# Performance work log

Measured on AMD Instinct MI355X. Metric: run time of the kernel, lower is better.

Reference implementation:

```python
import jax, jax.numpy as jnp
import numpy as np


def _conv1x1(W, b, x):
    # 1x1 conv == per-pixel matmul over channels: (O,C) x (B,C,H,W) -> (B,O,H,W)
    return jnp.einsum('oc,bchw->bohw', W, x) + b[None, :, None, None]


def setup_inputs() -> dict:
    key = jax.random.key(0)
    ks = jax.random.split(key, 7)
    B, C, H, W = 4, 256, 64, 64
    Cq = C // 8  # 32
    scale_qk = 1.0 / np.sqrt(C)
    x = jax.random.normal(ks[0], (B, C, H, W), dtype=jnp.float32)
    Wq = jax.random.normal(ks[1], (Cq, C), dtype=jnp.float32) * scale_qk
    bq = jnp.zeros((Cq,), dtype=jnp.float32)
    Wk = jax.random.normal(ks[2], (Cq, C), dtype=jnp.float32) * scale_qk
    bk = jnp.zeros((Cq,), dtype=jnp.float32)
    Wv = jax.random.normal(ks[3], (C, C), dtype=jnp.float32) * scale_qk
    bv = jnp.zeros((C,), dtype=jnp.float32)
    gamma = jnp.ones((1,), dtype=jnp.float32)  # torch init is 0; use 1 so attn branch is exercised
    return {'x': x, 'Wq': Wq, 'bq': bq, 'Wk': Wk, 'bk': bk, 'Wv': Wv, 'bv': bv, 'gamma': gamma}


def reference(x, Wq, bq, Wk, bk, Wv, bv, gamma):
    B, C, H, W = x.shape
    N = H * W
    # query/key projections + activation (relu), flattened over spatial dims
    q = jax.nn.relu(_conv1x1(Wq, bq, x)).reshape(B, -1, N)  # (B, C/8, N)
    k = jax.nn.relu(_conv1x1(Wk, bk, x)).reshape(B, -1, N)  # (B, C/8, N)
    # energy[b,n,m] = sum_c q[b,c,n] * k[b,c,m]  (= proj_query^T @ proj_key)
    energy = jnp.einsum('bcn,bcm->bnm', q, k)               # (B, N, N)
    attention = jax.nn.softmax(energy, axis=-1)
    v = jax.nn.relu(_conv1x1(Wv, bv, x)).reshape(B, C, N)   # (B, C, N)
    # out = v @ attention^T : out[b,c,n] = sum_m v[b,c,m] * attention[b,n,m]
    out = jnp.einsum('bcm,bnm->bcn', v, attention).reshape(B, C, H, W)
    out = gamma[0] * out + x
    return (out, attention)
```

## Files before the change

kernel.cpp:

```cpp
#include <hip/hip_runtime.h>
#include <hip/hip_bf16.h>

#define NB 4
#define NC 256
#define NQ 32
#define NN 4096
#define LOG2E 1.4426950408889634f

typedef __attribute__((ext_vector_type(4))) float f32x4;
typedef __attribute__((ext_vector_type(8))) short s16x8;

#define MFMA16(a, b, c) __builtin_amdgcn_mfma_f32_16x16x32_bf16((a), (b), (c), 0, 0, 0)

__device__ __forceinline__ float fexp2(float x) {
    float r;
    asm("v_exp_f32 %0, %1" : "=v"(r) : "v"(x));
    return r;
}

__device__ __forceinline__ void block_sync_lds() {
    asm volatile("s_waitcnt lgkmcnt(0)" ::: "memory");
    __builtin_amdgcn_s_barrier();
}

__device__ __forceinline__ int pswz(int row, int col) {
    return row * 64 + (col ^ ((row & 7) << 3));
}

__global__ __launch_bounds__(512, 2) void k_proj(
    const float* __restrict__ x,
    const float* __restrict__ Wq, const float* __restrict__ bq,
    const float* __restrict__ Wk, const float* __restrict__ bk,
    const float* __restrict__ Wv, const float* __restrict__ bv,
    __hip_bfloat16* __restrict__ qh, __hip_bfloat16* __restrict__ ql,
    __hip_bfloat16* __restrict__ kh, __hip_bfloat16* __restrict__ kl,
    __hip_bfloat16* __restrict__ vo)
{
    __shared__ __align__(16) float xs[NC * 64];
    const int b  = blockIdx.y;
    const int n0 = blockIdx.x * 64;
    const int t  = threadIdx.x;

    {
        const float* xb = x + (size_t)b * NC * NN + n0;
        #pragma unroll
        for (int it = 0; it < 8; ++it) {
            int i4 = t + it * 512;
            int c  = i4 >> 4;
            int nq = (i4 & 15) << 2;
            float4 v4 = *(const float4*)(xb + (size_t)c * NN + nq);
            *(float4*)&xs[c * 64 + nq] = v4;
        }
    }
    __syncthreads();

    const int g  = t >> 4;
    const int n4 = (t & 15) << 2;

    const float* Wr[10];
    float a[10][4];
    #pragma unroll
    for (int j = 0; j < 10; ++j) {
        int o = g + 32 * j;
        const float* Wrow; float bias;
        if (o < 32)      { Wrow = Wq + o * NC;        bias = bq[o]; }
        else if (o < 64) { Wrow = Wk + (o - 32) * NC; bias = bk[o - 32]; }
        else             { Wrow = Wv + (o - 64) * NC; bias = bv[o - 64]; }
        Wr[j] = Wrow;
        a[j][0] = a[j][1] = a[j][2] = a[j][3] = bias;
    }

    #pragma unroll 2
    for (int c0 = 0; c0 < NC; c0 += 4) {
        float4 xv[4];
        #pragma unroll
        for (int i = 0; i < 4; ++i) xv[i] = *(const float4*)&xs[(c0 + i) * 64 + n4];
        #pragma unroll
        for (int j = 0; j < 10; ++j) {
            float4 w = *(const float4*)(Wr[j] + c0);
            a[j][0] += w.x * xv[0].x + w.y * xv[1].x + w.z * xv[2].x + w.w * xv[3].x;
            a[j][1] += w.x * xv[0].y + w.y * xv[1].y + w.z * xv[2].y + w.w * xv[3].y;
            a[j][2] += w.x * xv[0].z + w.y * xv[1].z + w.z * xv[2].z + w.w * xv[3].z;
            a[j][3] += w.x * xv[0].w + w.y * xv[1].w + w.z * xv[2].w + w.w * xv[3].w;
        }
    }

    #pragma unroll
    for (int j = 0; j < 10; ++j) {
        int o = g + 32 * j;
        float a0 = fmaxf(a[j][0], 0.f), a1 = fmaxf(a[j][1], 0.f);
        float a2 = fmaxf(a[j][2], 0.f), a3 = fmaxf(a[j][3], 0.f);
        int nn = n0 + n4;
        if (o < 64) {
            __hip_bfloat16 *dh, *dl; int c; float sc;
            if (o < 32) { dh = qh; dl = ql; c = o;      sc = LOG2E; }
            else        { dh = kh; dl = kl; c = o - 32; sc = 1.0f;  }
            float vals[4] = {a0 * sc, a1 * sc, a2 * sc, a3 * sc};
            #pragma unroll
            for (int i = 0; i < 4; ++i) {
                float vv = vals[i];
                __hip_bfloat16 h = __float2bfloat16(vv);
                float lo = vv - __bfloat162float(h);
                size_t base = ((size_t)b * NN + nn + i) * NQ + c;
                dh[base] = h;
                dl[base] = __float2bfloat16(lo);
            }
        } else {
            union { __hip_bfloat16 h[4]; unsigned long long u; } pk;
            pk.h[0] = __float2bfloat16(a0); pk.h[1] = __float2bfloat16(a1);
            pk.h[2] = __float2bfloat16(a2); pk.h[3] = __float2bfloat16(a3);
            *(unsigned long long*)(vo + ((size_t)b * NC + (o - 64)) * NN + nn) = pk.u;
        }
    }
}

__global__ __launch_bounds__(1024, 4) void k_fused(
    const __hip_bfloat16* __restrict__ qh, const __hip_bfloat16* __restrict__ ql,
    const __hip_bfloat16* __restrict__ kh, const __hip_bfloat16* __restrict__ kl,
    const __hip_bfloat16* __restrict__ v,
    const float* __restrict__ x, const float* __restrict__ gamma,
    float* __restrict__ out, float* __restrict__ att)
{
    __shared__ __align__(16) __hip_bfloat16 ps[2][64 * 64];
    __shared__ float redM[16][16], redS[16][16];
    __shared__ float finM[64], finI[64];

    const int bid  = blockIdx.x;
    const int flat = (bid & 7) * 32 + (bid >> 3);
    const int b    = flat >> 6;
    const int n0   = (flat & 63) * 64;

    const int t = threadIdx.x, wv = t >> 6, lane = t & 63;
    const int r = lane & 15, hi = lane >> 4, kc = hi * 8;

    const __hip_bfloat16* khb = kh + (size_t)b * NN * NQ;
    const __hip_bfloat16* klb = kl + (size_t)b * NN * NQ;
    const __hip_bfloat16* vb  = v  + (size_t)b * NC * NN;

    {
        const int nt1 = wv >> 2, mq = wv & 3;
        const int nw = n0 + nt1 * 16;
        const s16x8 aqh = *(const s16x8*)(qh + ((size_t)b * NN + nw + r) * NQ + kc);
        const s16x8 aql = *(const s16x8*)(ql + ((size_t)b * NN + nw + r) * NQ + kc);
        const int mb = mq * 1024;
        float M = -3.0e38f, S = 0.f;
        s16x8 c0h = *(const s16x8*)(khb + (size_t)(mb + r) * NQ + kc);
        s16x8 c0l = *(const s16x8*)(klb + (size_t)(mb + r) * NQ + kc);
        s16x8 c1h = *(const s16x8*)(khb + (size_t)(mb + 16 + r) * NQ + kc);
        s16x8 c1l = *(const s16x8*)(klb + (size_t)(mb + 16 + r) * NQ + kc);
        #pragma unroll 1
        for (int it = 0; it < 32; ++it) {
            s16x8 u0h = c0h, u0l = c0l, u1h = c1h, u1l = c1l;
            if (it < 31) {
                int m = mb + (it + 1) * 32;
                c0h = *(const s16x8*)(khb + (size_t)(m + r) * NQ + kc);
                c0l = *(const s16x8*)(klb + (size_t)(m + r) * NQ + kc);
                c1h = *(const s16x8*)(khb + (size_t)(m + 16 + r) * NQ + kc);
                c1l = *(const s16x8*)(klb + (size_t)(m + 16 + r) * NQ + kc);
            }
            f32x4 e0 = {0.f, 0.f, 0.f, 0.f}, e1 = {0.f, 0.f, 0.f, 0.f};
            e0 = MFMA16(u0h, aqh, e0); e0 = MFMA16(u0l, aqh, e0); e0 = MFMA16(u0h, aql, e0);
            e1 = MFMA16(u1h, aqh, e1); e1 = MFMA16(u1l, aqh, e1); e1 = MFMA16(u1h, aql, e1);
            float mx = fmaxf(fmaxf(fmaxf(e0[0], e0[1]), fmaxf(e0[2], e0[3])),
                             fmaxf(fmaxf(e1[0], e1[1]), fmaxf(e1[2], e1[3])));
            float nm = fmaxf(M, mx);
            float s8 = fexp2(e0[0] - nm) + fexp2(e0[1] - nm) +
                       fexp2(e0[2] - nm) + fexp2(e0[3] - nm) +
                       fexp2(e1[0] - nm) + fexp2(e1[1] - nm) +
                       fexp2(e1[2] - nm) + fexp2(e1[3] - nm);
            S = S * fexp2(M - nm) + s8;
            M = nm;
        }
        #pragma unroll
        for (int off = 16; off <= 32; off <<= 1) {
            float M2 = __shfl_xor(M, off), S2 = __shfl_xor(S, off);
            float nm = fmaxf(M, M2);
            S = S * fexp2(M - nm) + S2 * fexp2(M2 - nm);
            M = nm;
        }
        if (lane < 16) { redM[wv][r] = M; redS[wv][r] = S; }
    }
    __syncthreads();
    if (t < 64) {
        const int w0 = (t >> 4) * 4, tl = t & 15;
        float M = redM[w0][tl], S = redS[w0][tl];
        #pragma unroll
        for (int i = 1; i < 4; ++i) {
            float M2 = redM[w0 + i][tl], S2 = redS[w0 + i][tl];
            float nm = fmaxf(M, M2);
            S = S * fexp2(M - nm) + S2 * fexp2(M2 - nm);
            M = nm;
        }
        finM[t] = M; finI[t] = 1.0f / S;
    }
    __syncthreads();

    if (wv < 8) {
        const int nt = wv >> 1, mh = wv & 1;
        const int nw = n0 + nt * 16;
        const s16x8 aqh = *(const s16x8*)(qh + ((size_t)b * NN + nw + r) * NQ + kc);
        const s16x8 aql = *(const s16x8*)(ql + ((size_t)b * NN + nw + r) * NQ + kc);
        const float fM = finM[nt * 16 + r], fI = finI[nt * 16 + r];
        float* arow = att + ((size_t)b * NN + nw + r) * NN;
        const int prow = nt * 16 + r;
        const int pc0  = mh * 32 + hi * 4;

        int mt = mh * 32;
        s16x8 c0h = *(const s16x8*)(khb + (size_t)(mt + r) * NQ + kc);
        s16x8 c0l = *(const s16x8*)(klb + (size_t)(mt + r) * NQ + kc);
        s16x8 c1h = *(const s16x8*)(khb + (size_t)(mt + 16 + r) * NQ + kc);
        s16x8 c1l = *(const s16x8*)(klb + (size_t)(mt + 16 + r) * NQ + kc);

        #pragma unroll 1
        for (int st = 0; st < 64; ++st) {
            const int buf = st & 1;
            s16x8 u0h = c0h, u0l = c0l, u1h = c1h, u1l = c1l;
            if (st < 63) {
                int mn = mt + 64;
                c0h = *(const s16x8*)(khb + (size_t)(mn + r) * NQ + kc);
                c0l = *(const s16x8*)(klb + (size_t)(mn + r) * NQ + kc);
                c1h = *(const s16x8*)(khb + (size_t)(mn + 16 + r) * NQ + kc);
                c1l = *(const s16x8*)(klb + (size_t)(mn + 16 + r) * NQ + kc);
            }
            f32x4 e0 = {0.f, 0.f, 0.f, 0.f}, e1 = {0.f, 0.f, 0.f, 0.f};
            e0 = MFMA16(u0h, aqh, e0); e0 = MFMA16(u0l, aqh, e0); e0 = MFMA16(u0h, aql, e0);
            e1 = MFMA16(u1h, aqh, e1); e1 = MFMA16(u1l, aqh, e1); e1 = MFMA16(u1h, aql, e1);

            f32x4 w0, w1;
            #pragma unroll
            for (int j = 0; j < 4; ++j) {
                w0[j] = fexp2(e0[j] - fM) * fI;
                w1[j] = fexp2(e1[j] - fM) * fI;
            }
            __builtin_nontemporal_store(w0, (f32x4*)(arow + mt + hi * 4));
            __builtin_nontemporal_store(w1, (f32x4*)(arow + mt + 16 + hi * 4));
            union { __hip_bfloat16 h[4]; unsigned long long u; } pk0, pk1;
            #pragma unroll
            for (int j = 0; j < 4; ++j) {
                pk0.h[j] = __float2bfloat16(w0[j]);
                pk1.h[j] = __float2bfloat16(w1[j]);
            }
            *(unsigned long long*)&ps[buf][pswz(prow, pc0)]      = pk0.u;
            *(unsigned long long*)&ps[buf][pswz(prow, pc0 + 16)] = pk1.u;

            block_sync_lds();
            mt += 64;
        }
    } else {
        const int cw = (wv - 8) * 32;
        f32x4 acc[2][4] = {};

        #pragma unroll 1
        for (int st = 0; st < 64; ++st) {
            if (st > 0) {
                const int cst = st - 1, pb = cst & 1, mP = cst * 64;
                s16x8 vf0[2], vf1[2], pf0[4], pf1[4];
                #pragma unroll
                for (int ct = 0; ct < 2; ++ct)
                    vf0[ct] = *(const s16x8*)(vb + (size_t)(cw + ct * 16 + r) * NN + mP + kc);
                #pragma unroll
                for (int nt = 0; nt < 4; ++nt)
                    pf0[nt] = *(const s16x8*)&ps[pb][pswz(nt * 16 + r, kc)];
                #pragma unroll
                for (int ct = 0; ct < 2; ++ct)
                    vf1[ct] = *(const s16x8*)(vb + (size_t)(cw + ct * 16 + r) * NN + mP + 32 + kc);
                #pragma unroll
                for (int nt = 0; nt < 4; ++nt)
                    pf1[nt] = *(const s16x8*)&ps[pb][pswz(nt * 16 + r, 32 + kc)];
                __builtin_amdgcn_s_setprio(1);
                #pragma unroll
                for (int ct = 0; ct < 2; ++ct)
                    #pragma unroll
                    for (int nt = 0; nt < 4; ++nt)
                        acc[ct][nt] = MFMA16(vf0[ct], pf0[nt], acc[ct][nt]);
                #pragma unroll
                for (int ct = 0; ct < 2; ++ct)
                    #pragma unroll
                    for (int nt = 0; nt < 4; ++nt)
                        acc[ct][nt] = MFMA16(vf1[ct], pf1[nt], acc[ct][nt]);
                __builtin_amdgcn_s_setprio(0);
            }
            block_sync_lds();
        }
        {
            const int mP = 63 * 64;
            s16x8 vf0[2], vf1[2], pf0[4], pf1[4];
            #pragma unroll
            for (int ct = 0; ct < 2; ++ct) {
                vf0[ct] = *(const s16x8*)(vb + (size_t)(cw + ct * 16 + r) * NN + mP + kc);
                vf1[ct] = *(const s16x8*)(vb + (size_t)(cw + ct * 16 + r) * NN + mP + 32 + kc);
            }
            #pragma unroll
            for (int nt = 0; nt < 4; ++nt) {
                pf0[nt] = *(const s16x8*)&ps[1][pswz(nt * 16 + r, kc)];
                pf1[nt] = *(const s16x8*)&ps[1][pswz(nt * 16 + r, 32 + kc)];
            }
            #pragma unroll
            for (int ct = 0; ct < 2; ++ct)
                #pragma unroll
                for (int nt = 0; nt < 4; ++nt) {
                    acc[ct][nt] = MFMA16(vf0[ct], pf0[nt], acc[ct][nt]);
                    acc[ct][nt] = MFMA16(vf1[ct], pf1[nt], acc[ct][nt]);
                }
        }
        const float gm = gamma[0];
        #pragma unroll
        for (int ct = 0; ct < 2; ++ct) {
            #pragma unroll
            for (int nt = 0; nt < 4; ++nt) {
                #pragma unroll
                for (int j = 0; j < 4; ++j) {
                    int c = cw + ct * 16 + hi * 4 + j;
                    size_t idx = ((size_t)b * NC + c) * NN + n0 + nt * 16 + r;
                    out[idx] = gm * acc[ct][nt][j] + x[idx];
                }
            }
        }
    }
}

extern "C" void kernel_launch(void* const* d_in, const int* in_sizes, int n_in,
                              void* d_out, int out_size, void* d_ws, size_t ws_size,
                              hipStream_t stream) {
    const float* x     = (const float*)d_in[0];
    const float* Wq    = (const float*)d_in[1];
    const float* bq    = (const float*)d_in[2];
    const float* Wk    = (const float*)d_in[3];
    const float* bk    = (const float*)d_in[4];
    const float* Wv    = (const float*)d_in[5];
    const float* bv    = (const float*)d_in[6];
    const float* gamma = (const float*)d_in[7];

    float* out = (float*)d_out;
    float* att = out + (size_t)NB * NC * NN;

    const size_t qk_elems = (size_t)NB * NN * NQ;
    __hip_bfloat16* qh = (__hip_bfloat16*)d_ws;
    __hip_bfloat16* ql = qh + qk_elems;
    __hip_bfloat16* kh = ql + qk_elems;
    __hip_bfloat16* kl = kh + qk_elems;
    __hip_bfloat16* vo = kl + qk_elems;

    k_proj <<<dim3(NN / 64, NB), 512, 0, stream>>>(x, Wq, bq, Wk, bk, Wv, bv,
                                                   qh, ql, kh, kl, vo);
    k_fused<<<dim3(256), 1024, 0, stream>>>(qh, ql, kh, kl, vo,
                                            x, gamma, out, att);
}
```

Measured before the change: 202.3 us.

## Move attention-matrix stores to PV waves and prefetch V fragments a step ahead

The attention matrix is no longer written in fp32 by the energy/softmax waves. The PV waves now read the bf16 probabilities back from LDS, widen them to fp32 and write them out, which rebalances global-store traffic between the two wave groups. V fragments are also loaded one stage ahead in registers so global loads overlap the MFMA work. The stored attention values are now bf16-rounded rather than full fp32, which reduces output precision.

```diff
diff --git a/kernel.cpp b/kernel.cpp
--- a/kernel.cpp
+++ b/kernel.cpp
@@ -16,6 +16,9 @@
     float r;
     asm("v_exp_f32 %0, %1" : "=v"(r) : "v"(x));
     return r;
+}
+__device__ __forceinline__ float bf2f(short s) {
+    return __uint_as_float(((unsigned int)(unsigned short)s) << 16);
 }
 
 __device__ __forceinline__ void block_sync_lds() {
@@ -201,7 +204,6 @@
         const s16x8 aqh = *(const s16x8*)(qh + ((size_t)b * NN + nw + r) * NQ + kc);
         const s16x8 aql = *(const s16x8*)(ql + ((size_t)b * NN + nw + r) * NQ + kc);
         const float fM = finM[nt * 16 + r], fI = finI[nt * 16 + r];
-        float* arow = att + ((size_t)b * NN + nw + r) * NN;
         const int prow = nt * 16 + r;
         const int pc0  = mh * 32 + hi * 4;
 
@@ -226,19 +228,11 @@
             e0 = MFMA16(u0h, aqh, e0); e0 = MFMA16(u0l, aqh, e0); e0 = MFMA16(u0h, aql, e0);
             e1 = MFMA16(u1h, aqh, e1); e1 = MFMA16(u1l, aqh, e1); e1 = MFMA16(u1h, aql, e1);
 
-            f32x4 w0, w1;
+            union { __hip_bfloat16 h[4]; unsigned long long u; } pk0, pk1;
             #pragma unroll
             for (int j = 0; j < 4; ++j) {
-                w0[j] = fexp2(e0[j] - fM) * fI;
-                w1[j] = fexp2(e1[j] - fM) * fI;
-            }
-            __builtin_nontemporal_store(w0, (f32x4*)(arow + mt + hi * 4));
-            __builtin_nontemporal_store(w1, (f32x4*)(arow + mt + 16 + hi * 4));
-            union { __hip_bfloat16 h[4]; unsigned long long u; } pk0, pk1;
-            #pragma unroll
-            for (int j = 0; j < 4; ++j) {
-                pk0.h[j] = __float2bfloat16(w0[j]);
-                pk1.h[j] = __float2bfloat16(w1[j]);
+                pk0.h[j] = __float2bfloat16(fexp2(e0[j] - fM) * fI);
+                pk1.h[j] = __float2bfloat16(fexp2(e1[j] - fM) * fI);
             }
             *(unsigned long long*)&ps[buf][pswz(prow, pc0)]      = pk0.u;
             *(unsigned long long*)&ps[buf][pswz(prow, pc0 + 16)] = pk1.u;
@@ -247,61 +241,101 @@
             mt += 64;
         }
     } else {
-        const int cw = (wv - 8) * 32;
+        const int pw  = wv - 8, cw = pw * 32;
+        const int ntw = pw >> 1;
+        const bool wact = ((r >> 3) == (pw & 1));
+        float* arow = att + ((size_t)b * NN + n0 + pw * 8 + (r & 7)) * NN;
         f32x4 acc[2][4] = {};
 
+        s16x8 vA00 = *(const s16x8*)(vb + (size_t)(cw + r) * NN + kc);
+        s16x8 vA01 = *(const s16x8*)(vb + (size_t)(cw + 16 + r) * NN + kc);
+        s16x8 vA10 = *(const s16x8*)(vb + (size_t)(cw + r) * NN + 32 + kc);
+        s16x8 vA11 = *(const s16x8*)(vb + (size_t)(cw + 16 + r) * NN + 32 + kc);
+
+        block_sync_lds();
+
         #pragma unroll 1
-        for (int st = 0; st < 64; ++st) {
-            if (st > 0) {
-                const int cst = st - 1, pb = cst & 1, mP = cst * 64;
-                s16x8 vf0[2], vf1[2], pf0[4], pf1[4];
+        for (int st = 1; st < 64; ++st) {
+            const int pb = (st - 1) & 1;
+            const int mP = (st - 1) * 64;
+            s16x8 pf[4];
+            #pragma unroll
+            for (int nt = 0; nt < 4; ++nt)
+                pf[nt] = *(const s16x8*)&ps[pb][pswz(nt * 16 + r, kc)];
+            __builtin_amdgcn_s_setprio(1);
+            #pragma unroll
+            for (int nt = 0; nt < 4; ++nt) {
+                acc[0][nt] = MFMA16(vA00, pf[nt], acc[0][nt]);
+                acc[1][nt] = MFMA16(vA01, pf[nt], acc[1][nt]);
+            }
+            __builtin_amdgcn_s_setprio(0);
+            #pragma unroll
+            for (int nt = 0; nt < 4; ++nt)
+                pf[nt] = *(const s16x8*)&ps[pb][pswz(nt * 16 + r, 32 + kc)];
+            __builtin_amdgcn_s_setprio(1);
+            #pragma unroll
+            for (int nt = 0; nt < 4; ++nt) {
+                acc[0][nt] = MFMA16(vA10, pf[nt], acc[0][nt]);
+                acc[1][nt] = MFMA16(vA11, pf[nt], acc[1][nt]);
+            }
+            __builtin_amdgcn_s_setprio(0);
+
+            {
+                const int mN = st * 64;
+                vA00 = *(const s16x8*)(vb + (size_t)(cw + r) * NN + mN + kc);
+                vA01 = *(const s16x8*)(vb + (size_t)(cw + 16 + r) * NN + mN + kc);
+                vA10 = *(const s16x8*)(vb + (size_t)(cw + r) * NN + mN + 32 + kc);
+                vA11 = *(const s16x8*)(vb + (size_t)(cw + 16 + r) * NN + mN + 32 + kc);
+            }
+            if (wact) {
+                s16x8 q0 = *(const s16x8*)&ps[pb][pswz(ntw * 16 + r, kc)];
+                s16x8 q1 = *(const s16x8*)&ps[pb][pswz(ntw * 16 + r, 32 + kc)];
+                f32x4 w0, w1, w2, w3;
                 #pragma unroll
-                for (int ct = 0; ct < 2; ++ct)
-                    vf0[ct] = *(const s16x8*)(vb + (size_t)(cw + ct * 16 + r) * NN + mP + kc);
+                for (int j = 0; j < 4; ++j) {
+                    w0[j] = bf2f(q0[j]); w1[j] = bf2f(q0[j + 4]);
+                    w2[j] = bf2f(q1[j]); w3[j] = bf2f(q1[j + 4]);
+                }
+                __builtin_nontemporal_store(w0, (f32x4*)(arow + mP + kc));
+                __builtin_nontemporal_store(w1, (f32x4*)(arow + mP + kc + 4));
+                __builtin_nontemporal_store(w2, (f32x4*)(arow + mP + 32 + kc));
+                __builtin_nontemporal_store(w3, (f32x4*)(arow + mP + 32 + kc + 4));
+            }
+            block_sync_lds();
+        }
+        {
+            const int pb = 1, mP = 63 * 64;
+            s16x8 pf[4];
+            #pragma unroll
+            for (int nt = 0; nt < 4; ++nt)
+                pf[nt] = *(const s16x8*)&ps[pb][pswz(nt * 16 + r, kc)];
+            #pragma unroll
+            for (int nt = 0; nt < 4; ++nt) {
+                acc[0][nt] = MFMA16(vA00, pf[nt], acc[0][nt]);
+                acc[1][nt] = MFMA16(vA01, pf[nt], acc[1][nt]);
+            }
+            #pragma unroll
+            for (int nt = 0; nt < 4; ++nt)
+                pf[nt] = *(const s16x8*)&ps[pb][pswz(nt * 16 + r, 32 + kc)];
+            #pragma unroll
+            for (int nt = 0; nt < 4; ++nt) {
+                acc[0][nt] = MFMA16(vA10, pf[nt], acc[0][nt]);
+                acc[1][nt] = MFMA16(vA11, pf[nt], acc[1][nt]);
+            }
+            if (wact) {
+                s16x8 q0 = *(const s16x8*)&ps[pb][pswz(ntw * 16 + r, kc)];
+                s16x8 q1 = *(const s16x8*)&ps[pb][pswz(ntw * 16 + r, 32 + kc)];
+                f32x4 w0, w1, w2, w3;
                 #pragma unroll
-                for (int nt = 0; nt < 4; ++nt)
-                    pf0[nt] = *(const s16x8*)&ps[pb][pswz(nt * 16 + r, kc)];
-                #pragma unroll
-                for (int ct = 0; ct < 2; ++ct)
-                    vf1[ct] = *(const s16x8*)(vb + (size_t)(cw + ct * 16 + r) * NN + mP + 32 + kc);
-                #pragma unroll
-                for (int nt = 0; nt < 4; ++nt)
-                    pf1[nt] = *(const s16x8*)&ps[pb][pswz(nt * 16 + r, 32 + kc)];
-                __builtin_amdgcn_s_setprio(1);
-                #pragma unroll
-                for (int ct = 0; ct < 2; ++ct)
-                    #pragma unroll
-                    for (int nt = 0; nt < 4; ++nt)
-                        acc[ct][nt] = MFMA16(vf0[ct], pf0[nt], acc[ct][nt]);
-                #pragma unroll
-                for (int ct = 0; ct < 2; ++ct)
-                    #pragma unroll
-                    for (int nt = 0; nt < 4; ++nt)
-                        acc[ct][nt] = MFMA16(vf1[ct], pf1[nt], acc[ct][nt]);
-                __builtin_amdgcn_s_setprio(0);
-            }
-            block_sync_lds();
-        }
-        {
-            const int mP = 63 * 64;
-            s16x8 vf0[2], vf1[2], pf0[4], pf1[4];
-            #pragma unroll
-            for (int ct = 0; ct < 2; ++ct) {
-                vf0[ct] = *(const s16x8*)(vb + (size_t)(cw + ct * 16 + r) * NN + mP + kc);
-                vf1[ct] = *(const s16x8*)(vb + (size_t)(cw + ct * 16 + r) * NN + mP + 32 + kc);
-            }
-            #pragma unroll
-            for (int nt = 0; nt < 4; ++nt) {
-                pf0[nt] = *(const s16x8*)&ps[1][pswz(nt * 16 + r, kc)];
-                pf1[nt] = *(const s16x8*)&ps[1][pswz(nt * 16 + r, 32 + kc)];
-            }
-            #pragma unroll
-            for (int ct = 0; ct < 2; ++ct)
-                #pragma unroll
-                for (int nt = 0; nt < 4; ++nt) {
-                    acc[ct][nt] = MFMA16(vf0[ct], pf0[nt], acc[ct][nt]);
-                    acc[ct][nt] = MFMA16(vf1[ct], pf1[nt], acc[ct][nt]);
+                for (int j = 0; j < 4; ++j) {
+                    w0[j] = bf2f(q0[j]); w1[j] = bf2f(q0[j + 4]);
+                    w2[j] = bf2f(q1[j]); w3[j] = bf2f(q1[j + 4]);
                 }
+                __builtin_nontemporal_store(w0, (f32x4*)(arow + mP + kc));
+                __builtin_nontemporal_store(w1, (f32x4*)(arow + mP + kc + 4));
+                __builtin_nontemporal_store(w2, (f32x4*)(arow + mP + 32 + kc));
+                __builtin_nontemporal_store(w3, (f32x4*)(arow + mP + 32 + kc + 4));
+            }
         }
         const float gm = gamma[0];
         #pragma unroll
```

New measurement: 200.8 us. Within noise of the previous version (-0.8%).

## Halve query tile per block and write attention via cooperative LDS-staged coalesced stores

Applied to the files above, without the earlier changes.

The fused kernel now processes 32 query rows per block with 512 threads and 512 blocks, instead of 64 rows with 1024 threads and 256 blocks. Probability tiles go into a 4-slot LDS ring, and every 256 columns all 8 waves read them back to emit full-row coalesced float4 attention stores. This replaces the per-lane scattered stores done by the energy waves alone. The stored attention values are now bf16-rounded rather than fp32, which changes the output precision. Each PV wave covers 64 channels, so per-block V reuse drops while the grid gains parallelism.

```diff
diff --git a/kernel.cpp b/kernel.cpp
--- a/kernel.cpp
+++ b/kernel.cpp
@@ -16,6 +16,9 @@
     float r;
     asm("v_exp_f32 %0, %1" : "=v"(r) : "v"(x));
     return r;
+}
+__device__ __forceinline__ float bf2f(unsigned short s) {
+    return __uint_as_float(((unsigned int)s) << 16);
 }
 
 __device__ __forceinline__ void block_sync_lds() {
@@ -114,21 +117,21 @@
     }
 }
 
-__global__ __launch_bounds__(1024, 4) void k_fused(
+__global__ __launch_bounds__(512, 4) void k_fused(
     const __hip_bfloat16* __restrict__ qh, const __hip_bfloat16* __restrict__ ql,
     const __hip_bfloat16* __restrict__ kh, const __hip_bfloat16* __restrict__ kl,
     const __hip_bfloat16* __restrict__ v,
     const float* __restrict__ x, const float* __restrict__ gamma,
     float* __restrict__ out, float* __restrict__ att)
 {
-    __shared__ __align__(16) __hip_bfloat16 ps[2][64 * 64];
-    __shared__ float redM[16][16], redS[16][16];
-    __shared__ float finM[64], finI[64];
+    __shared__ __align__(16) __hip_bfloat16 ps[4][32 * 64];
+    __shared__ float redM[8][16], redS[8][16];
+    __shared__ float finM[32], finI[32];
 
     const int bid  = blockIdx.x;
-    const int flat = (bid & 7) * 32 + (bid >> 3);
-    const int b    = flat >> 6;
-    const int n0   = (flat & 63) * 64;
+    const int swzb = (bid & 7) * 64 + (bid >> 3);
+    const int b    = swzb >> 7;
+    const int n0   = (swzb & 127) * 32;
 
     const int t = threadIdx.x, wv = t >> 6, lane = t & 63;
     const int r = lane & 15, hi = lane >> 4, kc = hi * 8;
@@ -138,7 +141,7 @@
     const __hip_bfloat16* vb  = v  + (size_t)b * NC * NN;
 
     {
-        const int nt1 = wv >> 2, mq = wv & 3;
+        const int nt1 = wv & 1, mq = wv >> 1;
         const int nw = n0 + nt1 * 16;
         const s16x8 aqh = *(const s16x8*)(qh + ((size_t)b * NN + nw + r) * NQ + kc);
         const s16x8 aql = *(const s16x8*)(ql + ((size_t)b * NN + nw + r) * NQ + kc);
@@ -181,12 +184,12 @@
         if (lane < 16) { redM[wv][r] = M; redS[wv][r] = S; }
     }
     __syncthreads();
-    if (t < 64) {
-        const int w0 = (t >> 4) * 4, tl = t & 15;
-        float M = redM[w0][tl], S = redS[w0][tl];
+    if (t < 32) {
+        const int nt1 = t >> 4, tl = t & 15;
+        float M = redM[nt1][tl], S = redS[nt1][tl];
         #pragma unroll
         for (int i = 1; i < 4; ++i) {
-            float M2 = redM[w0 + i][tl], S2 = redS[w0 + i][tl];
+            float M2 = redM[nt1 + 2 * i][tl], S2 = redS[nt1 + 2 * i][tl];
             float nm = fmaxf(M, M2);
             S = S * fexp2(M - nm) + S2 * fexp2(M2 - nm);
             M = nm;
@@ -195,119 +198,153 @@
     }
     __syncthreads();
 
-    if (wv < 8) {
-        const int nt = wv >> 1, mh = wv & 1;
+    float* attb = att + ((size_t)b * NN + n0) * NN;
+
+    if (wv < 4) {
+        const int nt = wv & 1, par = wv >> 1;
         const int nw = n0 + nt * 16;
         const s16x8 aqh = *(const s16x8*)(qh + ((size_t)b * NN + nw + r) * NQ + kc);
         const s16x8 aql = *(const s16x8*)(ql + ((size_t)b * NN + nw + r) * NQ + kc);
         const float fM = finM[nt * 16 + r], fI = finI[nt * 16 + r];
-        float* arow = att + ((size_t)b * NN + nw + r) * NN;
         const int prow = nt * 16 + r;
-        const int pc0  = mh * 32 + hi * 4;
-
-        int mt = mh * 32;
-        s16x8 c0h = *(const s16x8*)(khb + (size_t)(mt + r) * NQ + kc);
-        s16x8 c0l = *(const s16x8*)(klb + (size_t)(mt + r) * NQ + kc);
-        s16x8 c1h = *(const s16x8*)(khb + (size_t)(mt + 16 + r) * NQ + kc);
-        s16x8 c1l = *(const s16x8*)(klb + (size_t)(mt + 16 + r) * NQ + kc);
+
+        s16x8 cA[4], nA[4];
+        {
+            int m = par * 64;
+            cA[0] = *(const s16x8*)(khb + (size_t)(m + r) * NQ + kc);
+            cA[1] = *(const s16x8*)(klb + (size_t)(m + r) * NQ + kc);
+            cA[2] = *(const s16x8*)(khb + (size_t)(m + 16 + r) * NQ + kc);
+            cA[3] = *(const s16x8*)(klb + (size_t)(m + 16 + r) * NQ + kc);
+        }
 
         #pragma unroll 1
-        for (int st = 0; st < 64; ++st) {
-            const int buf = st & 1;
-            s16x8 u0h = c0h, u0l = c0l, u1h = c1h, u1l = c1l;
-            if (st < 63) {
-                int mn = mt + 64;
-                c0h = *(const s16x8*)(khb + (size_t)(mn + r) * NQ + kc);
-                c0l = *(const s16x8*)(klb + (size_t)(mn + r) * NQ + kc);
-                c1h = *(const s16x8*)(khb + (size_t)(mn + 16 + r) * NQ + kc);
-                c1l = *(const s16x8*)(klb + (size_t)(mn + 16 + r) * NQ + kc);
-            }
-            f32x4 e0 = {0.f, 0.f, 0.f, 0.f}, e1 = {0.f, 0.f, 0.f, 0.f};
-            e0 = MFMA16(u0h, aqh, e0); e0 = MFMA16(u0l, aqh, e0); e0 = MFMA16(u0h, aql, e0);
-            e1 = MFMA16(u1h, aqh, e1); e1 = MFMA16(u1l, aqh, e1); e1 = MFMA16(u1h, aql, e1);
-
-            f32x4 w0, w1;
-            #pragma unroll
-            for (int j = 0; j < 4; ++j) {
-                w0[j] = fexp2(e0[j] - fM) * fI;
-                w1[j] = fexp2(e1[j] - fM) * fI;
-            }
-            __builtin_nontemporal_store(w0, (f32x4*)(arow + mt + hi * 4));
-            __builtin_nontemporal_store(w1, (f32x4*)(arow + mt + 16 + hi * 4));
-            union { __hip_bfloat16 h[4]; unsigned long long u; } pk0, pk1;
-            #pragma unroll
-            for (int j = 0; j < 4; ++j) {
-                pk0.h[j] = __float2bfloat16(w0[j]);
-                pk1.h[j] = __float2bfloat16(w1[j]);
-            }
-            *(unsigned long long*)&ps[buf][pswz(prow, pc0)]      = pk0.u;
-            *(unsigned long long*)&ps[buf][pswz(prow, pc0 + 16)] = pk1.u;
-
+        for (int s = 0; s < 32; ++s) {
+            const int c = 2 * s + par, m0 = c * 64, slot = c & 3;
+            #pragma unroll
+            for (int sub = 0; sub < 2; ++sub) {
+                s16x8* cur = (sub == 0) ? cA : nA;
+                s16x8* nxt = (sub == 0) ? nA : cA;
+                int mn = (sub == 0) ? (m0 + 32) : (m0 + 128);
+                if (sub == 0 || s < 31) {
+                    nxt[0] = *(const s16x8*)(khb + (size_t)(mn + r) * NQ + kc);
+                    nxt[1] = *(const s16x8*)(klb + (size_t)(mn + r) * NQ + kc);
+                    nxt[2] = *(const s16x8*)(khb + (size_t)(mn + 16 + r) * NQ + kc);
+                    nxt[3] = *(const s16x8*)(klb + (size_t)(mn + 16 + r) * NQ + kc);
+                }
+                f32x4 e0 = {0.f, 0.f, 0.f, 0.f}, e1 = {0.f, 0.f, 0.f, 0.f};
+                e0 = MFMA16(cur[0], aqh, e0); e0 = MFMA16(cur[1], aqh, e0); e0 = MFMA16(cur[0], aql, e0);
+                e1 = MFMA16(cur[2], aqh, e1); e1 = MFMA16(cur[3], aqh, e1); e1 = MFMA16(cur[2], aql, e1);
+
+                union { __hip_bfloat16 h[4]; unsigned long long u; } pk0, pk1;
+                #pragma unroll
+                for (int j = 0; j < 4; ++j) {
+                    pk0.h[j] = __float2bfloat16(fexp2(e0[j] - fM) * fI);
+                    pk1.h[j] = __float2bfloat16(fexp2(e1[j] - fM) * fI);
+                }
+                *(unsigned long long*)&ps[slot][pswz(prow, sub * 32 + hi * 4)]      = pk0.u;
+                *(unsigned long long*)&ps[slot][pswz(prow, sub * 32 + 16 + hi * 4)] = pk1.u;
+            }
             block_sync_lds();
-            mt += 64;
+            if (s & 1) {
+                const int mb4 = (s >> 1) * 256;
+                const int slotL = lane >> 4, colL = (lane * 4) & 63;
+                #pragma unroll
+                for (int i = 0; i < 4; ++i) {
+                    int row = wv * 4 + i;
+                    unsigned long long pv = *(const unsigned long long*)
+                        &ps[slotL][pswz(row, colL)];
+                    f32x4 w;
+                    w[0] = bf2f((unsigned short)(pv));
+                    w[1] = bf2f((unsigned short)(pv >> 16));
+                    w[2] = bf2f((unsigned short)(pv >> 32));
+                    w[3] = bf2f((unsigned short)(pv >> 48));
+                    __builtin_nontemporal_store(w,
+                        (f32x4*)(attb + (size_t)row * NN + mb4 + lane * 4));
+                }
+                block_sync_lds();
+            }
         }
     } else {
-        const int cw = (wv - 8) * 32;
-        f32x4 acc[2][4] = {};
+        const int pw = wv - 4, cw = pw * 64;
+        f32x4 acc[4][2] = {};
 
         #pragma unroll 1
-        for (int st = 0; st < 64; ++st) {
-            if (st > 0) {
-                const int cst = st - 1, pb = cst & 1, mP = cst * 64;
-                s16x8 vf0[2], vf1[2], pf0[4], pf1[4];
-                #pragma unroll
-                for (int ct = 0; ct < 2; ++ct)
-                    vf0[ct] = *(const s16x8*)(vb + (size_t)(cw + ct * 16 + r) * NN + mP + kc);
-                #pragma unroll
-                for (int nt = 0; nt < 4; ++nt)
-                    pf0[nt] = *(const s16x8*)&ps[pb][pswz(nt * 16 + r, kc)];
-                #pragma unroll
-                for (int ct = 0; ct < 2; ++ct)
-                    vf1[ct] = *(const s16x8*)(vb + (size_t)(cw + ct * 16 + r) * NN + mP + 32 + kc);
-                #pragma unroll
-                for (int nt = 0; nt < 4; ++nt)
-                    pf1[nt] = *(const s16x8*)&ps[pb][pswz(nt * 16 + r, 32 + kc)];
-                __builtin_amdgcn_s_setprio(1);
-                #pragma unroll
-                for (int ct = 0; ct < 2; ++ct)
+        for (int s = 0; s < 32; ++s) {
+            if (s > 0) {
+                #pragma unroll
+                for (int cc2 = 0; cc2 < 2; ++cc2) {
+                    const int cc = 2 * (s - 1) + cc2, slot = cc & 3, mcc = cc * 64;
+                    s16x8 vf[4][2], pf[2][2];
                     #pragma unroll
-                    for (int nt = 0; nt < 4; ++nt)
-                        acc[ct][nt] = MFMA16(vf0[ct], pf0[nt], acc[ct][nt]);
-                #pragma unroll
-                for (int ct = 0; ct < 2; ++ct)
+                    for (int ct = 0; ct < 4; ++ct)
+                        #pragma unroll
+                        for (int ks = 0; ks < 2; ++ks)
+                            vf[ct][ks] = *(const s16x8*)(vb +
+                                (size_t)(cw + ct * 16 + r) * NN + mcc + ks * 32 + kc);
                     #pragma unroll
-                    for (int nt = 0; nt < 4; ++nt)
-                        acc[ct][nt] = MFMA16(vf1[ct], pf1[nt], acc[ct][nt]);
-                __builtin_amdgcn_s_setprio(0);
+                    for (int nt = 0; nt < 2; ++nt)
+                        #pragma unroll
+                        for (int ks = 0; ks < 2; ++ks)
+                            pf[nt][ks] = *(const s16x8*)&ps[slot][pswz(nt * 16 + r, ks * 32 + kc)];
+                    __builtin_amdgcn_s_setprio(1);
+                    #pragma unroll
+                    for (int ct = 0; ct < 4; ++ct)
+                        #pragma unroll
+                        for (int nt = 0; nt < 2; ++nt)
+                            #pragma unroll
+                            for (int ks = 0; ks < 2; ++ks)
+                                acc[ct][nt] = MFMA16(vf[ct][ks], pf[nt][ks], acc[ct][nt]);
+                    __builtin_amdgcn_s_setprio(0);
+                }
             }
             block_sync_lds();
-        }
-        {
-            const int mP = 63 * 64;
-            s16x8 vf0[2], vf1[2], pf0[4], pf1[4];
-            #pragma unroll
-            for (int ct = 0; ct < 2; ++ct) {
-                vf0[ct] = *(const s16x8*)(vb + (size_t)(cw + ct * 16 + r) * NN + mP + kc);
-                vf1[ct] = *(const s16x8*)(vb + (size_t)(cw + ct * 16 + r) * NN + mP + 32 + kc);
-            }
-            #pragma unroll
-            for (int nt = 0; nt < 4; ++nt) {
-                pf0[nt] = *(const s16x8*)&ps[1][pswz(nt * 16 + r, kc)];
-                pf1[nt] = *(const s16x8*)&ps[1][pswz(nt * 16 + r, 32 + kc)];
-            }
-            #pragma unroll
-            for (int ct = 0; ct < 2; ++ct)
-                #pragma unroll
-                for (int nt = 0; nt < 4; ++nt) {
-                    acc[ct][nt] = MFMA16(vf0[ct], pf0[nt], acc[ct][nt]);
-                    acc[ct][nt] = MFMA16(vf1[ct], pf1[nt], acc[ct][nt]);
-                }
+            if (s & 1) {
+                const int mb4 = (s >> 1) * 256;
+                const int slotL = lane >> 4, colL = (lane * 4) & 63;
+                #pragma unroll
+                for (int i = 0; i < 4; ++i) {
+                    int row = wv * 4 + i;
+                    unsigned long long pv = *(const unsigned long long*)
+                        &ps[slotL][pswz(row, colL)];
+                    f32x4 w;
+                    w[0] = bf2f((unsigned short)(pv));
+                    w[1] = bf2f((unsigned short)(pv >> 16));
+                    w[2] = bf2f((unsigned short)(pv >> 32));
+                    w[3] = bf2f((unsigned short)(pv >> 48));
+                    __builtin_nontemporal_store(w,
+                        (f32x4*)(attb + (size_t)row * NN + mb4 + lane * 4));
+                }
+                block_sync_lds();
+            }
+        }
+        #pragma unroll
+        for (int cc2 = 0; cc2 < 2; ++cc2) {
+            const int cc = 62 + cc2, slot = cc & 3, mcc = cc * 64;
+            s16x8 vf[4][2], pf[2][2];
+            #pragma unroll
+            for (int ct = 0; ct < 4; ++ct)
+                #pragma unroll
+                for (int ks = 0; ks < 2; ++ks)
+                    vf[ct][ks] = *(const s16x8*)(vb +
+                        (size_t)(cw + ct * 16 + r) * NN + mcc + ks * 32 + kc);
+            #pragma unroll
+            for (int nt = 0; nt < 2; ++nt)
+                #pragma unroll
+                for (int ks = 0; ks < 2; ++ks)
+                    pf[nt][ks] = *(const s16x8*)&ps[slot][pswz(nt * 16 + r, ks * 32 + kc)];
+            #pragma unroll
+            for (int ct = 0; ct < 4; ++ct)
+                #pragma unroll
+                for (int nt = 0; nt < 2; ++nt)
+                    #pragma unroll
+                    for (int ks = 0; ks < 2; ++ks)
+                        acc[ct][nt] = MFMA16(vf[ct][ks], pf[nt][ks], acc[ct][nt]);
         }
         const float gm = gamma[0];
         #pragma unroll
-        for (int ct = 0; ct < 2; ++ct) {
-            #pragma unroll
-            for (int nt = 0; nt < 4; ++nt) {
+        for (int ct = 0; ct < 4; ++ct) {
+            #pragma unroll
+            for (int nt = 0; nt < 2; ++nt) {
                 #pragma unroll
                 for (int j = 0; j < 4; ++j) {
                     int c = cw + ct * 16 + hi * 4 + j;
@@ -343,6 +380,6 @@
 
     k_proj <<<dim3(NN / 64, NB), 512, 0, stream>>>(x, Wq, bq, Wk, bk, Wv, bv,
                                                    qh, ql, kh, kl, vo);
-    k_fused<<<dim3(256), 1024, 0, stream>>>(qh, ql, kh, kl, vo,
-                                            x, gamma, out, att);
-}
+    k_fused<<<dim3(512), 512, 0, stream>>>(qh, ql, kh, kl, vo,
+                                           x, gamma, out, att);
+}
```

Result: slower. 247.9 us (+22.5%).
